# Kernel tuning notes

Hardware: AMD Instinct MI355X
Metric: run time of the kernel (lower is better)

## Reference

```python
import jax, jax.numpy as jnp
import numpy as np

DIM = 128
HEADS = 4
DIM_HEAD = 32
HIDDEN = HEADS * DIM_HEAD
SCALE = DIM_HEAD ** -0.5
EPS = 1e-5


def setup_inputs() -> dict:
    key = jax.random.key(0)
    ks = jax.random.split(key, 8)
    s = 1.0 / np.sqrt(DIM)
    x = jax.random.normal(ks[0], (32, DIM, 64, 64), dtype=jnp.float32)
    Wq = jax.random.uniform(ks[1], (HIDDEN, DIM), jnp.float32, -s, s)
    Wk = jax.random.uniform(ks[2], (HIDDEN, DIM), jnp.float32, -s, s)
    Wv = jax.random.uniform(ks[3], (HIDDEN, DIM), jnp.float32, -s, s)
    so = 1.0 / np.sqrt(HIDDEN)
    Wo = jax.random.uniform(ks[4], (DIM, HIDDEN), jnp.float32, -so, so)
    bo = jax.random.uniform(ks[5], (DIM,), jnp.float32, -so, so)
    gn_w = jnp.ones((DIM,), jnp.float32)
    gn_b = jnp.zeros((DIM,), jnp.float32)
    return {"x": x, "Wq": Wq, "Wk": Wk, "Wv": Wv, "Wo": Wo, "bo": bo,
            "gn_w": gn_w, "gn_b": gn_b}


def reference(x, Wq, Wk, Wv, Wo, bo, gn_w, gn_b):
    b, c, h, w = x.shape
    n = h * w
    xf = x.reshape(b, c, n)  # [b, c, n]
    # 1x1 convs (no bias) == channel matmuls; split heads: [b, H, d, n]
    def proj(W):
        return jnp.einsum('oc,bcn->bon', W, xf).reshape(b, HEADS, DIM_HEAD, n)
    q = proj(Wq)
    k = proj(Wk)
    v = proj(Wv)
    q = jax.nn.softmax(q, axis=-2) * SCALE  # softmax over head-dim d
    k = jax.nn.softmax(k, axis=-1)          # softmax over spatial n
    ctx = jnp.einsum('bhdn,bhen->bhde', k, v)   # [b,H,d,e], tiny d=e=32
    out = jnp.einsum('bhde,bhdn->bhen', ctx, q) # [b,H,e,n]
    out = out.reshape(b, HIDDEN, n)
    # output 1x1 conv with bias
    out = jnp.einsum('oc,bcn->bon', Wo, out) + bo[None, :, None]  # [b,dim,n]
    # GroupNorm(num_groups=1): normalize over (C, n) per sample
    mu = jnp.mean(out, axis=(1, 2), keepdims=True)
    var = jnp.var(out, axis=(1, 2), keepdims=True)
    out = (out - mu) * jax.lax.rsqrt(var + EPS)
    out = out * gn_w[None, :, None] + gn_b[None, :, None]
    return out.reshape(b, c, h, w)
```

## Files before the change

kernel.cpp:

```cpp
#include <hip/hip_runtime.h>


#define B_   32
#define C_   128
#define N_   4096
#define H_   4
#define D_   32
#define HID  128
#define NB   64
#define TPB  4
#define NSTRIP 16
#define STV  72
#define STA  136
#define SCALE 0.1767766952966369f
#define EPS  1e-5f

typedef __attribute__((ext_vector_type(8))) short short8;
typedef __attribute__((ext_vector_type(4))) short short4v;
typedef __attribute__((ext_vector_type(4))) float floatx4;

__device__ __forceinline__ short f2bf(float f) {
  unsigned u = __float_as_uint(f);
  u += 0x7FFFu + ((u >> 16) & 1u);
  return (short)(u >> 16);
}

#define XLOAD(tt)                                                        \
  _Pragma("unroll")                                                      \
  for (int nt = 0; nt < 4; ++nt)                                         \
    _Pragma("unroll")                                                    \
    for (int j = 0; j < 8; ++j)                                          \
      xr[nt][j] = xw[(size_t)j * N_ + (size_t)(tt) * NB + nt * 16];

#define XCVT(fragbuf)                                                    \
  _Pragma("unroll")                                                      \
  for (int nt = 0; nt < 4; ++nt) {                                       \
    short8 s;                                                            \
    _Pragma("unroll")                                                    \
    for (int j = 0; j < 8; ++j) s[j] = f2bf(xr[nt][j]);                  \
    *(short8*)&(fragbuf)[((w * 4 + nt) * 64 + L) * 8] = s;               \
  }

__global__ __launch_bounds__(256) void k_wcast(
    const float* __restrict__ Wq, const float* __restrict__ Wk,
    const float* __restrict__ Wv, const float* __restrict__ Wo,
    short* __restrict__ wb) {
  const int i = blockIdx.x * 256 + threadIdx.x;
  const float* srcs[4] = {Wq, Wk, Wv, Wo};
#pragma unroll
  for (int m = 0; m < 4; ++m) {
    floatx4 a = ((const floatx4*)srcs[m])[i];
    short4v s = { f2bf(a[0]), f2bf(a[1]), f2bf(a[2]), f2bf(a[3]) };
    ((short4v*)(wb + m * 16384))[i] = s;
  }
}

__global__ __launch_bounds__(256, 2) void k_kv_ctx(
    const float* __restrict__ x, const short* __restrict__ Wkb,
    const short* __restrict__ Wvb, float* __restrict__ ctx_u,
    float* __restrict__ Zsum) {
  __shared__ short frag[2][8192];
  __shared__ short ekbuf[C_ * STV];
  __shared__ short vbuf [C_ * STV];
  const int tid = threadIdx.x;
  const int w = tid >> 6, L = tid & 63, l15 = tid & 15, q4 = (tid & 63) >> 4;
  const int b = blockIdx.x / NSTRIP;
  const int strip = blockIdx.x % NSTRIP;
  const float* xw = x + (size_t)b * (C_ * N_) + (size_t)(w * 32 + q4 * 8) * N_
                      + (size_t)(strip * TPB) * NB + l15;

  short8 ak[2][4], av[2][4];
#pragma unroll
  for (int mt = 0; mt < 2; ++mt)
#pragma unroll
    for (int ks = 0; ks < 4; ++ks) {
      ak[mt][ks] = *(const short8*)&Wkb[(w * 32 + mt * 16 + l15) * C_ + ks * 32 + q4 * 8];
      av[mt][ks] = *(const short8*)&Wvb[(w * 32 + mt * 16 + l15) * C_ + ks * 32 + q4 * 8];
    }

  const floatx4 z4 = {0.f, 0.f, 0.f, 0.f};
  floatx4 ca[2][2] = {{z4, z4}, {z4, z4}};
  float zreg[2][4] = {{0.f,0.f,0.f,0.f},{0.f,0.f,0.f,0.f}};
  float xr[4][8];

  XLOAD(0)
  XCVT(frag[0])
  XLOAD(1)

  for (int t = 0; t < TPB; ++t) {
    __syncthreads();

    floatx4 acck[2][4], accv[2][4];
#pragma unroll
    for (int mt = 0; mt < 2; ++mt)
#pragma unroll
      for (int nt = 0; nt < 4; ++nt) { acck[mt][nt] = z4; accv[mt][nt] = z4; }
#pragma unroll
    for (int ks = 0; ks < 4; ++ks) {
      short8 Bf[4];
#pragma unroll
      for (int nt = 0; nt < 4; ++nt)
        Bf[nt] = *(const short8*)&frag[t & 1][((ks * 4 + nt) * 64 + L) * 8];
#pragma unroll
      for (int mt = 0; mt < 2; ++mt)
#pragma unroll
        for (int nt = 0; nt < 4; ++nt) {
          acck[mt][nt] = __builtin_amdgcn_mfma_f32_16x16x32_bf16(ak[mt][ks], Bf[nt], acck[mt][nt], 0, 0, 0);
          accv[mt][nt] = __builtin_amdgcn_mfma_f32_16x16x32_bf16(av[mt][ks], Bf[nt], accv[mt][nt], 0, 0, 0);
        }
    }

    if (t + 1 < TPB) {
      XCVT(frag[(t + 1) & 1])
      if (t + 2 < TPB) { XLOAD(t + 2) }
    }

#pragma unroll
    for (int mt = 0; mt < 2; ++mt)
#pragma unroll
      for (int nt = 0; nt < 4; ++nt)
#pragma unroll
        for (int r = 0; r < 4; ++r)
          acck[mt][nt][r] = __expf(acck[mt][nt][r]);
#pragma unroll
    for (int mt = 0; mt < 2; ++mt)
#pragma unroll
      for (int r = 0; r < 4; ++r)
        zreg[mt][r] += acck[mt][0][r] + acck[mt][1][r] + acck[mt][2][r] + acck[mt][3][r];
#pragma unroll
    for (int mt = 0; mt < 2; ++mt)
#pragma unroll
      for (int nt = 0; nt < 4; ++nt)
#pragma unroll
        for (int r = 0; r < 4; ++r) {
          ekbuf[(w * 32 + mt * 16 + q4 * 4 + r) * STV + nt * 16 + l15] = f2bf(acck[mt][nt][r]);
          vbuf [(w * 32 + mt * 16 + q4 * 4 + r) * STV + nt * 16 + l15] = f2bf(accv[mt][nt][r]);
        }

#pragma unroll
    for (int ks = 0; ks < 2; ++ks) {
      short8 ae[2], be[2];
#pragma unroll
      for (int mt = 0; mt < 2; ++mt)
        ae[mt] = *(const short8*)&ekbuf[(w * 32 + mt * 16 + l15) * STV + ks * 32 + q4 * 8];
#pragma unroll
      for (int nt = 0; nt < 2; ++nt)
        be[nt] = *(const short8*)&vbuf[(w * 32 + nt * 16 + l15) * STV + ks * 32 + q4 * 8];
#pragma unroll
      for (int mt = 0; mt < 2; ++mt)
#pragma unroll
        for (int nt = 0; nt < 2; ++nt)
          ca[mt][nt] = __builtin_amdgcn_mfma_f32_16x16x32_bf16(ae[mt], be[nt], ca[mt][nt], 0, 0, 0);
    }
  }

#pragma unroll
  for (int mt = 0; mt < 2; ++mt)
#pragma unroll
    for (int r = 0; r < 4; ++r) {
      float s = zreg[mt][r];
      s += __shfl_xor(s, 1); s += __shfl_xor(s, 2);
      s += __shfl_xor(s, 4); s += __shfl_xor(s, 8);
      if (l15 == 0) atomicAdd(&Zsum[b * HID + w * 32 + mt * 16 + q4 * 4 + r], s);
    }

  float* cb = &ctx_u[((size_t)b * H_ + w) * (D_ * D_)];
#pragma unroll
  for (int mt = 0; mt < 2; ++mt)
#pragma unroll
    for (int nt = 0; nt < 2; ++nt)
#pragma unroll
      for (int r = 0; r < 4; ++r)
        atomicAdd(&cb[(mt * 16 + q4 * 4 + r) * D_ + nt * 16 + l15], ca[mt][nt][r]);
}

__global__ __launch_bounds__(256, 2) void k_q_attn_o(
    const float* __restrict__ x, const short* __restrict__ Wqb,
    const short* __restrict__ Wob, const float* __restrict__ bo,
    const float* __restrict__ ctx_u, const float* __restrict__ Zsum,
    float* __restrict__ outp, float* __restrict__ stats) {
  __shared__ short frag[2][8192];
  __shared__ short qat[NB * STA];
  const int tid = threadIdx.x;
  const int w = tid >> 6, L = tid & 63, l15 = tid & 15, q4 = (tid & 63) >> 4;
  const int b = blockIdx.x / NSTRIP;
  const int strip = blockIdx.x % NSTRIP;
  const float* xw = x + (size_t)b * (C_ * N_) + (size_t)(w * 32 + q4 * 8) * N_
                      + (size_t)(strip * TPB) * NB + l15;

  float xr[4][8];
  XLOAD(0)
  XCVT(frag[0])
  XLOAD(1)

  short8 ae[2];
  {
    const float* cbase = ctx_u + (size_t)b * (H_ * D_ * D_) + w * 1024;
    const float* zbase = Zsum + b * HID + w * 32;
#pragma unroll
    for (int mt = 0; mt < 2; ++mt) {
      short8 s;
#pragma unroll
      for (int j = 0; j < 8; ++j) {
        const int d = q4 * 8 + j;
        float v = cbase[d * 32 + mt * 16 + l15] * __builtin_amdgcn_rcpf(zbase[d]);
        s[j] = f2bf(v);
      }
      ae[mt] = s;
    }
  }

  short8 aq[2][4], ao[2][4];
#pragma unroll
  for (int mt = 0; mt < 2; ++mt)
#pragma unroll
    for (int ks = 0; ks < 4; ++ks) {
      aq[mt][ks] = *(const short8*)&Wqb[(w * 32 + mt * 16 + l15) * C_ + ks * 32 + q4 * 8];
      ao[mt][ks] = *(const short8*)&Wob[(w * 32 + mt * 16 + l15) * HID + ks * 32 + q4 * 8];
    }

  const floatx4 z4 = {0.f, 0.f, 0.f, 0.f};
  float s1 = 0.f, s2 = 0.f;

  for (int t = 0; t < TPB; ++t) {
    const int n0 = (strip * TPB + t) * NB;
    __syncthreads();

    floatx4 acc[2][4];
#pragma unroll
    for (int mt = 0; mt < 2; ++mt)
#pragma unroll
      for (int nt = 0; nt < 4; ++nt) acc[mt][nt] = z4;
#pragma unroll
    for (int ks = 0; ks < 4; ++ks) {
      short8 Bf[4];
#pragma unroll
      for (int nt = 0; nt < 4; ++nt)
        Bf[nt] = *(const short8*)&frag[t & 1][((ks * 4 + nt) * 64 + L) * 8];
#pragma unroll
      for (int mt = 0; mt < 2; ++mt)
#pragma unroll
        for (int nt = 0; nt < 4; ++nt)
          acc[mt][nt] = __builtin_amdgcn_mfma_f32_16x16x32_bf16(aq[mt][ks], Bf[nt], acc[mt][nt], 0, 0, 0);
    }

    if (t + 1 < TPB) {
      XCVT(frag[(t + 1) & 1])
      if (t + 2 < TPB) { XLOAD(t + 2) }
    }

#pragma unroll
    for (int mt = 0; mt < 2; ++mt)
#pragma unroll
      for (int nt = 0; nt < 4; ++nt)
#pragma unroll
        for (int r = 0; r < 4; ++r)
          acc[mt][nt][r] = __expf(acc[mt][nt][r]);
    float inv[4];
#pragma unroll
    for (int nt = 0; nt < 4; ++nt) {
      float s = 0.f;
#pragma unroll
      for (int mt = 0; mt < 2; ++mt)
#pragma unroll
        for (int r = 0; r < 4; ++r) s += acc[mt][nt][r];
      s += __shfl_xor(s, 16); s += __shfl_xor(s, 32);
      inv[nt] = SCALE * __builtin_amdgcn_rcpf(s);
    }

#pragma unroll
    for (int mt = 0; mt < 2; ++mt)
#pragma unroll
      for (int nt = 0; nt < 4; ++nt) {
        short4v pk = { f2bf(acc[mt][nt][0] * inv[nt]), f2bf(acc[mt][nt][1] * inv[nt]),
                       f2bf(acc[mt][nt][2] * inv[nt]), f2bf(acc[mt][nt][3] * inv[nt]) };
        *(short4v*)&qat[(nt * 16 + l15) * STA + w * 32 + mt * 16 + q4 * 4] = pk;
      }

    {
      floatx4 aacc[2][4];
#pragma unroll
      for (int mt = 0; mt < 2; ++mt)
#pragma unroll
        for (int nt = 0; nt < 4; ++nt) aacc[mt][nt] = z4;
#pragma unroll
      for (int nt = 0; nt < 4; ++nt) {
        short8 bq = *(const short8*)&qat[(nt * 16 + l15) * STA + w * 32 + q4 * 8];
#pragma unroll
        for (int mt = 0; mt < 2; ++mt)
          aacc[mt][nt] = __builtin_amdgcn_mfma_f32_16x16x32_bf16(ae[mt], bq, aacc[mt][nt], 0, 0, 0);
      }
#pragma unroll
      for (int nt = 0; nt < 4; ++nt)
#pragma unroll
        for (int mt = 0; mt < 2; ++mt) {
          short4v pk = { f2bf(aacc[mt][nt][0]), f2bf(aacc[mt][nt][1]),
                         f2bf(aacc[mt][nt][2]), f2bf(aacc[mt][nt][3]) };
          *(short4v*)&qat[(nt * 16 + l15) * STA + w * 32 + mt * 16 + q4 * 4] = pk;
        }
    }
    __syncthreads();

    floatx4 oacc[2][4];
#pragma unroll
    for (int mt = 0; mt < 2; ++mt)
#pragma unroll
      for (int nt = 0; nt < 4; ++nt) oacc[mt][nt] = z4;
#pragma unroll
    for (int ks = 0; ks < 4; ++ks) {
      short8 bf8[4];
#pragma unroll
      for (int nt = 0; nt < 4; ++nt)
        bf8[nt] = *(const short8*)&qat[(nt * 16 + l15) * STA + ks * 32 + q4 * 8];
#pragma unroll
      for (int mt = 0; mt < 2; ++mt)
#pragma unroll
        for (int nt = 0; nt < 4; ++nt)
          oacc[mt][nt] = __builtin_amdgcn_mfma_f32_16x16x32_bf16(ao[mt][ks], bf8[nt], oacc[mt][nt], 0, 0, 0);
    }

#pragma unroll
    for (int mt = 0; mt < 2; ++mt) {
      const int rowbase = w * 32 + mt * 16 + q4 * 4;
      const floatx4 bo4 = *(const floatx4*)&bo[rowbase];
#pragma unroll
      for (int nt = 0; nt < 4; ++nt) {
        const int n = n0 + nt * 16 + l15;
#pragma unroll
        for (int r = 0; r < 4; ++r) {
          float vv = oacc[mt][nt][r] + bo4[r];
          outp[(size_t)b * (C_ * N_) + (size_t)(rowbase + r) * N_ + n] = vv;
          s1 += vv; s2 += vv * vv;
        }
      }
    }
  }

#pragma unroll
  for (int m = 1; m < 64; m <<= 1) {
    s1 += __shfl_xor(s1, m);
    s2 += __shfl_xor(s2, m);
  }
  if ((tid & 63) == 0) {
    atomicAdd(&stats[b * 2 + 0], s1);
    atomicAdd(&stats[b * 2 + 1], s2);
  }
}

__global__ __launch_bounds__(256) void k_gnorm(
    float* __restrict__ outp, const float* __restrict__ stats,
    const float* __restrict__ gnw, const float* __restrict__ gnb) {
  const int b = blockIdx.x >> 6;
  const int blk = blockIdx.x & 63;
  const float M = (float)(C_ * N_);
  const float mu = stats[b * 2 + 0] / M;
  const float var = stats[b * 2 + 1] / M - mu * mu;
  const float rs = rsqrtf(var + EPS);
  floatx4* p = (floatx4*)(outp + (size_t)b * (C_ * N_) + (size_t)blk * 8192);
  const int tid = threadIdx.x;
#pragma unroll
  for (int i = 0; i < 8; ++i) {
    const int idx = tid + i * 256;
    const int fl = blk * 8192 + idx * 4;
    const int c = fl >> 12;
    const float wgt = gnw[c] * rs;
    const float bia = gnb[c] - mu * wgt;
    floatx4 v = p[idx];
    v[0] = v[0] * wgt + bia;
    v[1] = v[1] * wgt + bia;
    v[2] = v[2] * wgt + bia;
    v[3] = v[3] * wgt + bia;
    p[idx] = v;
  }
}

extern "C" void kernel_launch(void* const* d_in, const int* in_sizes, int n_in,
                              void* d_out, int out_size, void* d_ws, size_t ws_size,
                              hipStream_t stream) {
  (void)in_sizes; (void)n_in; (void)out_size; (void)ws_size;
  const float* x   = (const float*)d_in[0];
  const float* Wq  = (const float*)d_in[1];
  const float* Wk  = (const float*)d_in[2];
  const float* Wv  = (const float*)d_in[3];
  const float* Wo  = (const float*)d_in[4];
  const float* bo  = (const float*)d_in[5];
  const float* gnw = (const float*)d_in[6];
  const float* gnb = (const float*)d_in[7];
  float* outp  = (float*)d_out;
  float* ctx_u = (float*)d_ws;
  float* Zsum  = ctx_u + B_ * H_ * D_ * D_;
  float* stats = Zsum + B_ * HID;
  short* wb    = (short*)(stats + B_ * 2);
  const size_t zbytes = (size_t)(B_ * H_ * D_ * D_ + B_ * HID + B_ * 2) * sizeof(float);
  hipMemsetAsync(d_ws, 0, zbytes, stream);
  hipLaunchKernelGGL(k_wcast,    dim3(64),          dim3(256), 0, stream, Wq, Wk, Wv, Wo, wb);
  hipLaunchKernelGGL(k_kv_ctx,   dim3(B_ * NSTRIP), dim3(256), 0, stream, x, wb + 16384, wb + 32768, ctx_u, Zsum);
  hipLaunchKernelGGL(k_q_attn_o, dim3(B_ * NSTRIP), dim3(256), 0, stream, x, wb, wb + 49152, bo, ctx_u, Zsum, outp, stats);
  hipLaunchKernelGGL(k_gnorm,    dim3(B_ * 64),     dim3(256), 0, stream, outp, stats, gnw, gnb);
}
```

Measured before the change: 196.1 us.

## Cache bf16 x fragments in workspace and stream them into LDS via global_load_lds

The first kernel now also writes its bf16-converted x fragments to a workspace buffer. The second kernel stops re-reading fp32 x and converting it, and instead copies the prepacked bf16 tiles straight into LDS with direct global-to-LDS loads, double-buffered across tiles. Output stores become nontemporal. This halves the second pass's x read bytes and drops its conversion work, at the cost of an extra bf16 write in the first kernel and a dependence on workspace size and offset.

```diff
diff --git a/kernel.cpp b/kernel.cpp
--- a/kernel.cpp
+++ b/kernel.cpp
@@ -24,6 +24,11 @@
   u += 0x7FFFu + ((u >> 16) & 1u);
   return (short)(u >> 16);
 }
+__device__ __forceinline__ void gload_lds16(const float* g, void* l) {
+  __builtin_amdgcn_global_load_lds(
+      (const __attribute__((address_space(1))) unsigned int*)g,
+      (__attribute__((address_space(3))) unsigned int*)l, 16, 0, 0);
+}
 
 #define XLOAD(tt)                                                        \
   _Pragma("unroll")                                                      \
@@ -32,14 +37,22 @@
     for (int j = 0; j < 8; ++j)                                          \
       xr[nt][j] = xw[(size_t)j * N_ + (size_t)(tt) * NB + nt * 16];
 
-#define XCVT(fragbuf)                                                    \
+#define XCVTS(fragbuf, tt)                                               \
+  { short* xg_ = xt + ((size_t)(blockIdx.x * TPB + (tt))) * 8192;        \
   _Pragma("unroll")                                                      \
   for (int nt = 0; nt < 4; ++nt) {                                       \
     short8 s;                                                            \
     _Pragma("unroll")                                                    \
     for (int j = 0; j < 8; ++j) s[j] = f2bf(xr[nt][j]);                  \
     *(short8*)&(fragbuf)[((w * 4 + nt) * 64 + L) * 8] = s;               \
-  }
+    *(short8*)&xg_[((w * 4 + nt) * 64 + L) * 8] = s;                     \
+  } }
+
+#define GLDS(dstbuf, tt)                                                 \
+  { const float* src_ = (const float*)(xt + ((size_t)(blockIdx.x * TPB + (tt))) * 8192); \
+  _Pragma("unroll")                                                      \
+  for (int i = 0; i < 4; ++i)                                            \
+    gload_lds16(src_ + tid * 4 + i * 1024, (char*)(dstbuf) + tid * 16 + i * 4096); }
 
 __global__ __launch_bounds__(256) void k_wcast(
     const float* __restrict__ Wq, const float* __restrict__ Wk,
@@ -58,7 +71,7 @@
 __global__ __launch_bounds__(256, 2) void k_kv_ctx(
     const float* __restrict__ x, const short* __restrict__ Wkb,
     const short* __restrict__ Wvb, float* __restrict__ ctx_u,
-    float* __restrict__ Zsum) {
+    float* __restrict__ Zsum, short* __restrict__ xt) {
   __shared__ short frag[2][8192];
   __shared__ short ekbuf[C_ * STV];
   __shared__ short vbuf [C_ * STV];
@@ -84,7 +97,7 @@
   float xr[4][8];
 
   XLOAD(0)
-  XCVT(frag[0])
+  XCVTS(frag[0], 0)
   XLOAD(1)
 
   for (int t = 0; t < TPB; ++t) {
@@ -111,7 +124,7 @@
     }
 
     if (t + 1 < TPB) {
-      XCVT(frag[(t + 1) & 1])
+      XCVTS(frag[(t + 1) & 1], t + 1)
       if (t + 2 < TPB) { XLOAD(t + 2) }
     }
 
@@ -175,7 +188,7 @@
 }
 
 __global__ __launch_bounds__(256, 2) void k_q_attn_o(
-    const float* __restrict__ x, const short* __restrict__ Wqb,
+    const short* __restrict__ xt, const short* __restrict__ Wqb,
     const short* __restrict__ Wob, const float* __restrict__ bo,
     const float* __restrict__ ctx_u, const float* __restrict__ Zsum,
     float* __restrict__ outp, float* __restrict__ stats) {
@@ -185,13 +198,9 @@
   const int w = tid >> 6, L = tid & 63, l15 = tid & 15, q4 = (tid & 63) >> 4;
   const int b = blockIdx.x / NSTRIP;
   const int strip = blockIdx.x % NSTRIP;
-  const float* xw = x + (size_t)b * (C_ * N_) + (size_t)(w * 32 + q4 * 8) * N_
-                      + (size_t)(strip * TPB) * NB + l15;
-
-  float xr[4][8];
-  XLOAD(0)
-  XCVT(frag[0])
-  XLOAD(1)
+
+  GLDS(frag[0], 0)
+  GLDS(frag[1], 1)
 
   short8 ae[2];
   {
@@ -244,11 +253,6 @@
           acc[mt][nt] = __builtin_amdgcn_mfma_f32_16x16x32_bf16(aq[mt][ks], Bf[nt], acc[mt][nt], 0, 0, 0);
     }
 
-    if (t + 1 < TPB) {
-      XCVT(frag[(t + 1) & 1])
-      if (t + 2 < TPB) { XLOAD(t + 2) }
-    }
-
 #pragma unroll
     for (int mt = 0; mt < 2; ++mt)
 #pragma unroll
@@ -301,6 +305,8 @@
     }
     __syncthreads();
 
+    if (t + 2 < TPB) { GLDS(frag[t & 1], t + 2) }
+
     floatx4 oacc[2][4];
 #pragma unroll
     for (int mt = 0; mt < 2; ++mt)
@@ -329,7 +335,8 @@
 #pragma unroll
         for (int r = 0; r < 4; ++r) {
           float vv = oacc[mt][nt][r] + bo4[r];
-          outp[(size_t)b * (C_ * N_) + (size_t)(rowbase + r) * N_ + n] = vv;
+          __builtin_nontemporal_store(vv,
+              &outp[(size_t)b * (C_ * N_) + (size_t)(rowbase + r) * N_ + n]);
           s1 += vv; s2 += vv * vv;
         }
       }
@@ -391,10 +398,11 @@
   float* Zsum  = ctx_u + B_ * H_ * D_ * D_;
   float* stats = Zsum + B_ * HID;
   short* wb    = (short*)(stats + B_ * 2);
+  short* xt    = (short*)((char*)d_ws + 672000);
   const size_t zbytes = (size_t)(B_ * H_ * D_ * D_ + B_ * HID + B_ * 2) * sizeof(float);
   hipMemsetAsync(d_ws, 0, zbytes, stream);
   hipLaunchKernelGGL(k_wcast,    dim3(64),          dim3(256), 0, stream, Wq, Wk, Wv, Wo, wb);
-  hipLaunchKernelGGL(k_kv_ctx,   dim3(B_ * NSTRIP), dim3(256), 0, stream, x, wb + 16384, wb + 32768, ctx_u, Zsum);
-  hipLaunchKernelGGL(k_q_attn_o, dim3(B_ * NSTRIP), dim3(256), 0, stream, x, wb, wb + 49152, bo, ctx_u, Zsum, outp, stats);
+  hipLaunchKernelGGL(k_kv_ctx,   dim3(B_ * NSTRIP), dim3(256), 0, stream, x, wb + 16384, wb + 32768, ctx_u, Zsum, xt);
+  hipLaunchKernelGGL(k_q_attn_o, dim3(B_ * NSTRIP), dim3(256), 0, stream, xt, wb, wb + 49152, bo, ctx_u, Zsum, outp, stats);
   hipLaunchKernelGGL(k_gnorm,    dim3(B_ * 64),     dim3(256), 0, stream, outp, stats, gnw, gnb);
 }
```

After: 204.8 us. 1.04x slower.
